# Optimization experiments

Measured on AMD Instinct MI355X. Metric: run time of the kernel, lower is better.

The kernel has to match this reference:

```python
import jax, jax.numpy as jnp
import numpy as np

B, NM, D, H = 16384, 5, 256, 8
LN_EPS = 1e-5


def _ln(x, g, b):
    m = jnp.mean(x, axis=-1, keepdims=True)
    v = jnp.var(x, axis=-1, keepdims=True)
    return (x - m) / jnp.sqrt(v + LN_EPS) * g + b


def _mha(q_in, kv_in, Wi, bi, Wo, bo):
    # q_in: [B,1,D], kv_in: [B,1,D]; Wi: [3D,D] packed q/k/v like nn.MultiheadAttention
    Bq, Lq, Dm = q_in.shape
    Lk = kv_in.shape[1]
    dh = Dm // H
    q = (q_in @ Wi[:Dm].T + bi[:Dm]).reshape(Bq, Lq, H, dh).transpose(0, 2, 1, 3)
    k = (kv_in @ Wi[Dm:2 * Dm].T + bi[Dm:2 * Dm]).reshape(Bq, Lk, H, dh).transpose(0, 2, 1, 3)
    v = (kv_in @ Wi[2 * Dm:].T + bi[2 * Dm:]).reshape(Bq, Lk, H, dh).transpose(0, 2, 1, 3)
    scores = jnp.einsum('bhqd,bhkd->bhqk', q, k) * (1.0 / np.sqrt(dh))
    attn = jax.nn.softmax(scores, axis=-1)  # trivially 1.0 for Lk=1, kept for fidelity
    out = jnp.einsum('bhqk,bhkd->bhqd', attn, v).transpose(0, 2, 1, 3).reshape(Bq, Lq, Dm)
    return out @ Wo.T + bo


def setup_inputs() -> dict:
    key = jax.random.key(0)
    ks = jax.random.split(key, 8)
    s = 0.02
    return {
        'x': jax.random.normal(ks[0], (B, NM, D), jnp.float32),
        'self_Wi': jax.random.normal(ks[1], (3 * D, D), jnp.float32) * s,
        'self_bi': jnp.zeros((3 * D,), jnp.float32),
        'self_Wo': jax.random.normal(ks[2], (D, D), jnp.float32) * s,
        'self_bo': jnp.zeros((D,), jnp.float32),
        'cross_Wi': jax.random.normal(ks[3], (4, 3 * D, D), jnp.float32) * s,
        'cross_bi': jnp.zeros((4, 3 * D), jnp.float32),
        'cross_Wo': jax.random.normal(ks[4], (4, D, D), jnp.float32) * s,
        'cross_bo': jnp.zeros((4, D), jnp.float32),
        'cross_ln_g': jnp.ones((4, D), jnp.float32),
        'cross_ln_b': jnp.zeros((4, D), jnp.float32),
        'gate_ln_g': jnp.ones((D,), jnp.float32),
        'gate_ln_b': jnp.zeros((D,), jnp.float32),
        'gate_W': jax.random.normal(ks[5], (NM, D), jnp.float32) * s,
        'gate_b': jnp.zeros((NM,), jnp.float32),
        'final_ln_g': jnp.ones((D,), jnp.float32),
        'final_ln_b': jnp.zeros((D,), jnp.float32),
        'modal_idx': 2,
    }


def reference(x, self_Wi, self_bi, self_Wo, self_bo,
              cross_Wi, cross_bi, cross_Wo, cross_bo, cross_ln_g, cross_ln_b,
              gate_ln_g, gate_ln_b, gate_W, gate_b, final_ln_g, final_ln_b,
              modal_idx):
    query = x[:, modal_idx:modal_idx + 1, :]  # [B,1,D]
    self_out = _mha(query, query, self_Wi, self_bi, self_Wo, self_bo)

    other_idx = [i for i in range(NM) if i != modal_idx]
    kv = jnp.swapaxes(x[:, other_idx, :], 0, 1)[:, :, None, :]  # [4,B,1,D]

    def branch(Wi, bi, Wo, bo, g, b, kv_i):
        a = _mha(query, kv_i, Wi, bi, Wo, bo)
        return _ln(query + a, g, b)  # dropout is identity in eval

    cross_outs = jax.vmap(branch)(cross_Wi, cross_bi, cross_Wo, cross_bo,
                                  cross_ln_g, cross_ln_b, kv)  # [4,B,1,D]

    gates = jax.nn.softmax(_ln(query, gate_ln_g, gate_ln_b) @ gate_W.T + gate_b, axis=-1)  # [B,1,5]
    combined = gates[..., 0:1] * self_out + jnp.einsum('nbld,bln->bld', cross_outs, gates[..., 1:])
    return _ln(query + combined, final_ln_g, final_ln_b)
```

## Files before the change

kernel.cpp:

```cpp
#include <hip/hip_runtime.h>


typedef __attribute__((ext_vector_type(8))) short short8;
typedef __attribute__((ext_vector_type(4))) float floatx4;

__device__ __forceinline__ float b2f(unsigned short h) {
    union { unsigned int u; float f; } v; v.u = ((unsigned int)h) << 16; return v.f;
}
__device__ __forceinline__ unsigned short f2b(float f) {
    union { unsigned int u; float f; } v; v.f = f;
    unsigned int u = v.u;
    return (unsigned short)((u + 0x7FFFu + ((u >> 16) & 1u)) >> 16);
}

__global__ __launch_bounds__(256) void k_fuse(
    const float* __restrict__ sWi, const float* __restrict__ sbi,
    const float* __restrict__ sWo, const float* __restrict__ sbo,
    const float* __restrict__ cWi, const float* __restrict__ cbi,
    const float* __restrict__ cWo, const float* __restrict__ cbo,
    unsigned short* __restrict__ WT, float* __restrict__ BF)
{
    int s = blockIdx.y;
    int i0 = blockIdx.x * 4;
    int tid = threadIdx.x;
    const float *Wo, *Wv, *bv, *bo;
    if (s == 0) { Wo = sWo; Wv = sWi + 512 * 256; bv = sbi + 512; bo = sbo; }
    else {
        int n = s - 1;
        Wo = cWo + n * 65536;
        Wv = cWi + n * 768 * 256 + 512 * 256;
        bv = cbi + n * 768 + 512;
        bo = cbo + n * 256;
    }
    __shared__ float wo[4 * 256];
    #pragma unroll
    for (int it = 0; it < 4; ++it) {
        int idx = tid + it * 256;
        wo[idx] = Wo[i0 * 256 + idx];
    }
    __syncthreads();
    float a0 = 0.f, a1 = 0.f, a2 = 0.f, a3 = 0.f;
    #pragma unroll 8
    for (int k = 0; k < 256; ++k) {
        float wv = Wv[k * 256 + tid];
        a0 += wo[k] * wv;
        a1 += wo[256 + k] * wv;
        a2 += wo[512 + k] * wv;
        a3 += wo[768 + k] * wv;
    }
    {
        unsigned short vals[4] = { f2b(a0), f2b(a1), f2b(a2), f2b(a3) };
        int kk = tid >> 5, q4k = (tid >> 3) & 3, e = tid & 7;
        #pragma unroll
        for (int r = 0; r < 4; ++r) {
            int n = i0 + r;
            int w = n >> 5, ct = (n >> 4) & 1, l16n = n & 15;
            size_t idx = (((((((size_t)s * 8 + kk) * 8 + w) * 2 + ct) * 4 + q4k) * 16 + l16n) * 8) + e;
            WT[idx] = vals[r];
        }
    }
    {
        int wv_ = tid >> 6, ln = tid & 63;
        float p = 0.f;
        #pragma unroll
        for (int u = 0; u < 4; ++u) {
            int k = ln * 4 + u;
            p += wo[wv_ * 256 + k] * bv[k];
        }
        #pragma unroll
        for (int o = 32; o > 0; o >>= 1) p += __shfl_xor(p, o, 64);
        if (ln == 0) BF[s * 256 + i0 + wv_] = p + bo[i0 + wv_];
    }
}

__device__ __forceinline__ float wred(float v) {
    #pragma unroll
    for (int o = 32; o > 0; o >>= 1) v += __shfl_xor(v, o, 64);
    return v;
}

#define ASTR 264

__global__ __launch_bounds__(256, 3) void k_main(
    const float* __restrict__ x, const unsigned short* __restrict__ WT,
    const float* __restrict__ BF,
    const float* __restrict__ cln_g, const float* __restrict__ cln_b,
    const float* __restrict__ gln_g, const float* __restrict__ gln_b,
    const float* __restrict__ gW, const float* __restrict__ gb,
    const float* __restrict__ fln_g, const float* __restrict__ fln_b,
    const int* __restrict__ midx, float* __restrict__ out)
{
    __shared__ __align__(16) unsigned short Axl[5][16 * ASTR];
    __shared__ float gLDS[16 * 8];

    const int m = midx[0];
    const int b0 = blockIdx.x * 16;
    const int tid = threadIdx.x;
    const int wave = tid >> 6, lane = tid & 63;
    const int l16 = lane & 15, q4 = lane >> 4;
    const int j = lane * 4;

    float4 sreg[5][4];
    #pragma unroll
    for (int mi = 0; mi < 5; ++mi) {
        int mod = (mi == 0) ? m : ((mi - 1 < m) ? mi - 1 : mi);
        #pragma unroll
        for (int it = 0; it < 4; ++it) {
            int c = tid + it * 256;
            sreg[mi][it] = *(const float4*)(x + ((size_t)(b0 + (c >> 6)) * 5 + mod) * 256 + ((c & 63) << 2));
        }
    }

    float qv[4][4];
    #pragma unroll
    for (int rr = 0; rr < 4; ++rr) {
        int r = wave * 4 + rr;
        float4 u = *(const float4*)(x + ((size_t)(b0 + r) * 5 + m) * 256 + j);
        qv[rr][0] = u.x; qv[rr][1] = u.y; qv[rr][2] = u.z; qv[rr][3] = u.w;
    }
    float4 glg = *(const float4*)(gln_g + j);
    float4 glb = *(const float4*)(gln_b + j);
    float gbv[5];
    #pragma unroll
    for (int n = 0; n < 5; ++n) gbv[n] = gb[n];

    #pragma unroll
    for (int rr = 0; rr < 4; ++rr) {
        int r = wave * 4 + rr;
        float s1 = wred(qv[rr][0] + qv[rr][1] + qv[rr][2] + qv[rr][3]);
        float s2 = wred(qv[rr][0]*qv[rr][0] + qv[rr][1]*qv[rr][1] +
                        qv[rr][2]*qv[rr][2] + qv[rr][3]*qv[rr][3]);
        float mn = s1 * (1.f / 256.f);
        float vr = s2 * (1.f / 256.f) - mn * mn;
        float rs = rsqrtf(vr + 1e-5f);
        float qln[4];
        qln[0] = (qv[rr][0] - mn) * rs * glg.x + glb.x;
        qln[1] = (qv[rr][1] - mn) * rs * glg.y + glb.y;
        qln[2] = (qv[rr][2] - mn) * rs * glg.z + glb.z;
        qln[3] = (qv[rr][3] - mn) * rs * glg.w + glb.w;
        float g[5];
        #pragma unroll
        for (int n = 0; n < 5; ++n) {
            float4 w4 = *(const float4*)(gW + n * 256 + j);
            float p = qln[0] * w4.x + qln[1] * w4.y + qln[2] * w4.z + qln[3] * w4.w;
            g[n] = wred(p) + gbv[n];
        }
        float mx = g[0];
        #pragma unroll
        for (int n = 1; n < 5; ++n) mx = fmaxf(mx, g[n]);
        float es = 0.f;
        #pragma unroll
        for (int n = 0; n < 5; ++n) { g[n] = __expf(g[n] - mx); es += g[n]; }
        float inv = 1.f / es;
        if (lane == 0) {
            #pragma unroll
            for (int n = 0; n < 5; ++n) gLDS[r * 8 + n] = g[n] * inv;
        }
    }

    #pragma unroll
    for (int mi = 0; mi < 5; ++mi) {
        #pragma unroll
        for (int it = 0; it < 4; ++it) {
            int c = tid + it * 256;
            float4 v = sreg[mi][it];
            uint2 p;
            p.x = (unsigned int)f2b(v.x) | ((unsigned int)f2b(v.y) << 16);
            p.y = (unsigned int)f2b(v.z) | ((unsigned int)f2b(v.w) << 16);
            *(uint2*)(&Axl[mi][(c >> 6) * ASTR + ((c & 63) << 2)]) = p;
        }
    }
    __syncthreads();

    float comb[4][4];
    #pragma unroll
    for (int rr = 0; rr < 4; ++rr)
        #pragma unroll
        for (int i = 0; i < 4; ++i) comb[rr][i] = 0.f;

    for (int s = 0; s < 5; ++s) {
        float4 bfv = *(const float4*)(BF + s * 256 + j);
        float4 cg, cb;
        if (s > 0) {
            cg = *(const float4*)(cln_g + (s - 1) * 256 + j);
            cb = *(const float4*)(cln_b + (s - 1) * 256 + j);
        }

        floatx4 acc[4];
        #pragma unroll
        for (int ct = 0; ct < 4; ++ct) acc[ct] = (floatx4){0.f, 0.f, 0.f, 0.f};
        const unsigned short* wT = WT + (size_t)s * 65536;
        const unsigned short* As = &Axl[s][0];
        #pragma unroll
        for (int h = 0; h < 4; ++h) {
            short8 bb[8];
            #pragma unroll
            for (int kk2 = 0; kk2 < 2; ++kk2) {
                int kkg = h * 2 + kk2;
                #pragma unroll
                for (int ct = 0; ct < 4; ++ct) {
                    int wp = wave * 2 + (ct >> 1), ctp = ct & 1;
                    bb[kk2 * 4 + ct] = *(const short8*)(
                        wT + (((((size_t)kkg * 8 + wp) * 2 + ctp) * 4 + q4) * 16 + l16) * 8);
                }
            }
            #pragma unroll
            for (int kk2 = 0; kk2 < 2; ++kk2) {
                int k = (h * 2 + kk2) * 32 + q4 * 8;
                short8 a = *(const short8*)(&As[l16 * ASTR + k]);
                #pragma unroll
                for (int ct = 0; ct < 4; ++ct)
                    acc[ct] = __builtin_amdgcn_mfma_f32_16x16x32_bf16(a, bb[kk2 * 4 + ct], acc[ct], 0, 0, 0);
            }
        }
        __syncthreads();

        #pragma unroll
        for (int i = 0; i < 4; ++i) {
            int r = q4 * 4 + i;
            #pragma unroll
            for (int ct = 0; ct < 4; ++ct)
                Axl[s][r * ASTR + wave * 64 + ct * 16 + l16] = f2b(acc[ct][i]);
        }
        __syncthreads();

        if (s == 0) {
            #pragma unroll
            for (int rr = 0; rr < 4; ++rr) {
                int r = wave * 4 + rr;
                uint2 u = *(const uint2*)(&Axl[s][r * ASTR + j]);
                float y0 = b2f(u.x & 0xffff) + bfv.x, y1 = b2f(u.x >> 16) + bfv.y;
                float y2 = b2f(u.y & 0xffff) + bfv.z, y3 = b2f(u.y >> 16) + bfv.w;
                float g0 = gLDS[r * 8 + 0];
                comb[rr][0] += g0 * y0; comb[rr][1] += g0 * y1;
                comb[rr][2] += g0 * y2; comb[rr][3] += g0 * y3;
            }
        } else {
            #pragma unroll
            for (int rr = 0; rr < 4; ++rr) {
                int r = wave * 4 + rr;
                uint2 u = *(const uint2*)(&Axl[s][r * ASTR + j]);
                float t0 = qv[rr][0] + b2f(u.x & 0xffff) + bfv.x;
                float t1 = qv[rr][1] + b2f(u.x >> 16)    + bfv.y;
                float t2 = qv[rr][2] + b2f(u.y & 0xffff) + bfv.z;
                float t3 = qv[rr][3] + b2f(u.y >> 16)    + bfv.w;
                float s1 = wred(t0 + t1 + t2 + t3);
                float s2 = wred(t0*t0 + t1*t1 + t2*t2 + t3*t3);
                float mn = s1 * (1.f / 256.f);
                float vr = s2 * (1.f / 256.f) - mn * mn;
                float rs = rsqrtf(vr + 1e-5f);
                float gs = gLDS[r * 8 + s];
                comb[rr][0] += gs * ((t0 - mn) * rs * cg.x + cb.x);
                comb[rr][1] += gs * ((t1 - mn) * rs * cg.y + cb.y);
                comb[rr][2] += gs * ((t2 - mn) * rs * cg.z + cb.z);
                comb[rr][3] += gs * ((t3 - mn) * rs * cg.w + cb.w);
            }
        }
    }

    float4 fg = *(const float4*)(fln_g + j);
    float4 fb = *(const float4*)(fln_b + j);
    #pragma unroll
    for (int rr = 0; rr < 4; ++rr) {
        int r = wave * 4 + rr;
        float t0 = qv[rr][0] + comb[rr][0], t1 = qv[rr][1] + comb[rr][1];
        float t2 = qv[rr][2] + comb[rr][2], t3 = qv[rr][3] + comb[rr][3];
        float s1 = wred(t0 + t1 + t2 + t3);
        float s2 = wred(t0*t0 + t1*t1 + t2*t2 + t3*t3);
        float mn = s1 * (1.f / 256.f);
        float vr = s2 * (1.f / 256.f) - mn * mn;
        float rs = rsqrtf(vr + 1e-5f);
        float4 ov;
        ov.x = (t0 - mn) * rs * fg.x + fb.x;
        ov.y = (t1 - mn) * rs * fg.y + fb.y;
        ov.z = (t2 - mn) * rs * fg.z + fb.z;
        ov.w = (t3 - mn) * rs * fg.w + fb.w;
        *(float4*)(out + (size_t)(b0 + r) * 256 + j) = ov;
    }
}

extern "C" void kernel_launch(void* const* d_in, const int* in_sizes, int n_in,
                              void* d_out, int out_size, void* d_ws, size_t ws_size,
                              hipStream_t stream) {
    const float* x    = (const float*)d_in[0];
    const float* sWi  = (const float*)d_in[1];
    const float* sbi  = (const float*)d_in[2];
    const float* sWo  = (const float*)d_in[3];
    const float* sbo  = (const float*)d_in[4];
    const float* cWi  = (const float*)d_in[5];
    const float* cbi  = (const float*)d_in[6];
    const float* cWo  = (const float*)d_in[7];
    const float* cbo  = (const float*)d_in[8];
    const float* clng = (const float*)d_in[9];
    const float* clnb = (const float*)d_in[10];
    const float* glng = (const float*)d_in[11];
    const float* glnb = (const float*)d_in[12];
    const float* gW   = (const float*)d_in[13];
    const float* gb   = (const float*)d_in[14];
    const float* flng = (const float*)d_in[15];
    const float* flnb = (const float*)d_in[16];
    const int* midx   = (const int*)d_in[17];
    float* out        = (float*)d_out;

    char* ws = (char*)d_ws;
    unsigned short* WT = (unsigned short*)ws;
    float* BF          = (float*)(ws + 655360);

    k_fuse<<<dim3(64, 5), 256, 0, stream>>>(sWi, sbi, sWo, sbo, cWi, cbi, cWo, cbo, WT, BF);
    k_main<<<1024, 256, 0, stream>>>(x, WT, BF, clng, clnb, glng, glnb, gW, gb, flng, flnb, midx, out);
}
```

Measured before the change: 214.5 us.

## Swizzle LDS tiles, keep gates in registers, split x loads, raise occupancy

```diff
diff --git a/kernel.cpp b/kernel.cpp
--- a/kernel.cpp
+++ b/kernel.cpp
@@ -40,7 +40,6 @@
     }
     __syncthreads();
     float a0 = 0.f, a1 = 0.f, a2 = 0.f, a3 = 0.f;
-    #pragma unroll 8
     for (int k = 0; k < 256; ++k) {
         float wv = Wv[k * 256 + tid];
         a0 += wo[k] * wv;
@@ -79,9 +78,9 @@
     return v;
 }
 
-#define ASTR 264
-
-__global__ __launch_bounds__(256, 3) void k_main(
+#define SWZ(r, c) ((c) ^ (((r) & 7) << 3))
+
+__global__ __launch_bounds__(256, 4) void k_main(
     const float* __restrict__ x, const unsigned short* __restrict__ WT,
     const float* __restrict__ BF,
     const float* __restrict__ cln_g, const float* __restrict__ cln_b,
@@ -90,8 +89,7 @@
     const float* __restrict__ fln_g, const float* __restrict__ fln_b,
     const int* __restrict__ midx, float* __restrict__ out)
 {
-    __shared__ __align__(16) unsigned short Axl[5][16 * ASTR];
-    __shared__ float gLDS[16 * 8];
+    __shared__ __align__(16) unsigned short Axl[5][16 * 256];
 
     const int m = midx[0];
     const int b0 = blockIdx.x * 16;
@@ -100,17 +98,6 @@
     const int l16 = lane & 15, q4 = lane >> 4;
     const int j = lane * 4;
 
-    float4 sreg[5][4];
-    #pragma unroll
-    for (int mi = 0; mi < 5; ++mi) {
-        int mod = (mi == 0) ? m : ((mi - 1 < m) ? mi - 1 : mi);
-        #pragma unroll
-        for (int it = 0; it < 4; ++it) {
-            int c = tid + it * 256;
-            sreg[mi][it] = *(const float4*)(x + ((size_t)(b0 + (c >> 6)) * 5 + mod) * 256 + ((c & 63) << 2));
-        }
-    }
-
     float qv[4][4];
     #pragma unroll
     for (int rr = 0; rr < 4; ++rr) {
@@ -120,13 +107,21 @@
     }
     float4 glg = *(const float4*)(gln_g + j);
     float4 glb = *(const float4*)(gln_b + j);
-    float gbv[5];
-    #pragma unroll
-    for (int n = 0; n < 5; ++n) gbv[n] = gb[n];
-
+
+    float4 sr[5][4];
+    #pragma unroll
+    for (int mi = 0; mi < 3; ++mi) {
+        int mod = (mi == 0) ? m : ((mi - 1 < m) ? mi - 1 : mi);
+        #pragma unroll
+        for (int it = 0; it < 4; ++it) {
+            int c = tid + it * 256;
+            sr[mi][it] = *(const float4*)(x + ((size_t)(b0 + (c >> 6)) * 5 + mod) * 256 + ((c & 63) << 2));
+        }
+    }
+
+    float gt[4][5];
     #pragma unroll
     for (int rr = 0; rr < 4; ++rr) {
-        int r = wave * 4 + rr;
         float s1 = wred(qv[rr][0] + qv[rr][1] + qv[rr][2] + qv[rr][3]);
         float s2 = wred(qv[rr][0]*qv[rr][0] + qv[rr][1]*qv[rr][1] +
                         qv[rr][2]*qv[rr][2] + qv[rr][3]*qv[rr][3]);
@@ -143,7 +138,7 @@
         for (int n = 0; n < 5; ++n) {
             float4 w4 = *(const float4*)(gW + n * 256 + j);
             float p = qln[0] * w4.x + qln[1] * w4.y + qln[2] * w4.z + qln[3] * w4.w;
-            g[n] = wred(p) + gbv[n];
+            g[n] = wred(p) + gb[n];
         }
         float mx = g[0];
         #pragma unroll
@@ -152,22 +147,31 @@
         #pragma unroll
         for (int n = 0; n < 5; ++n) { g[n] = __expf(g[n] - mx); es += g[n]; }
         float inv = 1.f / es;
-        if (lane == 0) {
-            #pragma unroll
-            for (int n = 0; n < 5; ++n) gLDS[r * 8 + n] = g[n] * inv;
-        }
-    }
-
-    #pragma unroll
-    for (int mi = 0; mi < 5; ++mi) {
+        #pragma unroll
+        for (int n = 0; n < 5; ++n) gt[rr][n] = g[n] * inv;
+    }
+
+    #pragma unroll
+    for (int mi = 3; mi < 5; ++mi) {
+        int mod = (mi - 1 < m) ? mi - 1 : mi;
         #pragma unroll
         for (int it = 0; it < 4; ++it) {
             int c = tid + it * 256;
-            float4 v = sreg[mi][it];
+            sr[mi][it] = *(const float4*)(x + ((size_t)(b0 + (c >> 6)) * 5 + mod) * 256 + ((c & 63) << 2));
+        }
+    }
+    #pragma unroll
+    for (int mi = 0; mi < 5; ++mi) {
+        #pragma unroll
+        for (int it = 0; it < 4; ++it) {
+            int c = tid + it * 256;
+            int row = c >> 6;
+            int cs = (c & 63) << 2;
+            float4 v = sr[mi][it];
             uint2 p;
             p.x = (unsigned int)f2b(v.x) | ((unsigned int)f2b(v.y) << 16);
             p.y = (unsigned int)f2b(v.z) | ((unsigned int)f2b(v.w) << 16);
-            *(uint2*)(&Axl[mi][(c >> 6) * ASTR + ((c & 63) << 2)]) = p;
+            *(uint2*)(&Axl[mi][row * 256 + SWZ(row, cs)]) = p;
         }
     }
     __syncthreads();
@@ -178,6 +182,7 @@
         #pragma unroll
         for (int i = 0; i < 4; ++i) comb[rr][i] = 0.f;
 
+    #pragma unroll
     for (int s = 0; s < 5; ++s) {
         float4 bfv = *(const float4*)(BF + s * 256 + j);
         float4 cg, cb;
@@ -190,28 +195,20 @@
         #pragma unroll
         for (int ct = 0; ct < 4; ++ct) acc[ct] = (floatx4){0.f, 0.f, 0.f, 0.f};
         const unsigned short* wT = WT + (size_t)s * 65536;
-        const unsigned short* As = &Axl[s][0];
-        #pragma unroll
-        for (int h = 0; h < 4; ++h) {
-            short8 bb[8];
-            #pragma unroll
-            for (int kk2 = 0; kk2 < 2; ++kk2) {
-                int kkg = h * 2 + kk2;
-                #pragma unroll
-                for (int ct = 0; ct < 4; ++ct) {
-                    int wp = wave * 2 + (ct >> 1), ctp = ct & 1;
-                    bb[kk2 * 4 + ct] = *(const short8*)(
-                        wT + (((((size_t)kkg * 8 + wp) * 2 + ctp) * 4 + q4) * 16 + l16) * 8);
-                }
+        #pragma unroll
+        for (int h = 0; h < 8; ++h) {
+            short8 bb[4];
+            #pragma unroll
+            for (int ct = 0; ct < 4; ++ct) {
+                int wp = wave * 2 + (ct >> 1), ctp = ct & 1;
+                bb[ct] = *(const short8*)(
+                    wT + (((((size_t)h * 8 + wp) * 2 + ctp) * 4 + q4) * 16 + l16) * 8);
             }
-            #pragma unroll
-            for (int kk2 = 0; kk2 < 2; ++kk2) {
-                int k = (h * 2 + kk2) * 32 + q4 * 8;
-                short8 a = *(const short8*)(&As[l16 * ASTR + k]);
-                #pragma unroll
-                for (int ct = 0; ct < 4; ++ct)
-                    acc[ct] = __builtin_amdgcn_mfma_f32_16x16x32_bf16(a, bb[kk2 * 4 + ct], acc[ct], 0, 0, 0);
-            }
+            int k = h * 32 + q4 * 8;
+            short8 a = *(const short8*)(&Axl[s][l16 * 256 + SWZ(l16, k)]);
+            #pragma unroll
+            for (int ct = 0; ct < 4; ++ct)
+                acc[ct] = __builtin_amdgcn_mfma_f32_16x16x32_bf16(a, bb[ct], acc[ct], 0, 0, 0);
         }
         __syncthreads();
 
@@ -220,7 +217,7 @@
             int r = q4 * 4 + i;
             #pragma unroll
             for (int ct = 0; ct < 4; ++ct)
-                Axl[s][r * ASTR + wave * 64 + ct * 16 + l16] = f2b(acc[ct][i]);
+                Axl[s][r * 256 + SWZ(r, wave * 64 + ct * 16 + l16)] = f2b(acc[ct][i]);
         }
         __syncthreads();
 
@@ -228,10 +225,10 @@
             #pragma unroll
             for (int rr = 0; rr < 4; ++rr) {
                 int r = wave * 4 + rr;
-                uint2 u = *(const uint2*)(&Axl[s][r * ASTR + j]);
+                uint2 u = *(const uint2*)(&Axl[s][r * 256 + SWZ(r, j)]);
                 float y0 = b2f(u.x & 0xffff) + bfv.x, y1 = b2f(u.x >> 16) + bfv.y;
                 float y2 = b2f(u.y & 0xffff) + bfv.z, y3 = b2f(u.y >> 16) + bfv.w;
-                float g0 = gLDS[r * 8 + 0];
+                float g0 = gt[rr][0];
                 comb[rr][0] += g0 * y0; comb[rr][1] += g0 * y1;
                 comb[rr][2] += g0 * y2; comb[rr][3] += g0 * y3;
             }
@@ -239,7 +236,7 @@
             #pragma unroll
             for (int rr = 0; rr < 4; ++rr) {
                 int r = wave * 4 + rr;
-                uint2 u = *(const uint2*)(&Axl[s][r * ASTR + j]);
+                uint2 u = *(const uint2*)(&Axl[s][r * 256 + SWZ(r, j)]);
                 float t0 = qv[rr][0] + b2f(u.x & 0xffff) + bfv.x;
                 float t1 = qv[rr][1] + b2f(u.x >> 16)    + bfv.y;
                 float t2 = qv[rr][2] + b2f(u.y & 0xffff) + bfv.z;
@@ -249,7 +246,7 @@
                 float mn = s1 * (1.f / 256.f);
                 float vr = s2 * (1.f / 256.f) - mn * mn;
                 float rs = rsqrtf(vr + 1e-5f);
-                float gs = gLDS[r * 8 + s];
+                float gs = gt[rr][s];
                 comb[rr][0] += gs * ((t0 - mn) * rs * cg.x + cb.x);
                 comb[rr][1] += gs * ((t1 - mn) * rs * cg.y + cb.y);
                 comb[rr][2] += gs * ((t2 - mn) * rs * cg.z + cb.z);
```

New measurement: 290.5 us. +35.4%, slower.
